# Performance work log

Measured on AMD Instinct MI355X. Metric: run time of the kernel, lower is better.

The kernel has to match this reference:

```python
import jax, jax.numpy as jnp
import numpy as np

BIG = 1e6  # sentinel 'no zero pixel found yet' distance; BIG**2 = 1e12 fits fp32


def _edt(is_fg):
    """Exact Euclidean distance transform (scipy.distance_transform_edt semantics):
    distance from each nonzero pixel to the nearest zero pixel. is_fg: [N,H,W] bool.
    Separable exact algorithm: 1D vertical distance-to-zero per column via cummax
    scans, then min-plus convolution with the parabola (j-k)^2 along rows."""
    N, H, W = is_fg.shape
    is_zero = ~is_fg
    ih = jnp.arange(H, dtype=jnp.float32)[None, :, None]
    # nearest zero at-or-above / at-or-below along H (per column)
    up = jax.lax.cummax(jnp.where(is_zero, ih, -BIG), axis=1)
    dn = -jax.lax.cummax(jnp.where(is_zero, -ih, -BIG), axis=1, reverse=True)
    g = jnp.minimum(ih - up, dn - ih)               # [N,H,W] vertical 1D distance
    g2 = jnp.minimum(g, BIG) ** 2
    ks = jnp.arange(W, dtype=jnp.float32)
    def col(j):
        # exact 2D squared distance for output column j: min_k (j-k)^2 + g(.,.,k)^2
        return jnp.min((j.astype(jnp.float32) - ks) ** 2 + g2, axis=-1)  # [N,H]
    d2 = jax.lax.map(col, jnp.arange(W))            # [W,N,H], sequential -> low memory
    return jnp.sqrt(jnp.moveaxis(d2, 0, -1))        # [N,H,W]


def setup_inputs() -> dict:
    key = jax.random.key(0)
    k1, k2 = jax.random.split(key)
    B, C, H, W = 8, 12, 256, 256
    logits = jax.random.normal(k1, (B, C, H, W), dtype=jnp.float32)
    targets = jax.random.randint(k2, (B, H, W), 0, C, dtype=jnp.int32)
    return {"logits": logits, "targets": targets}


def reference(logits, targets):
    B, C, H, W = logits.shape
    probs = jax.nn.softmax(logits, axis=1)                                  # [B,C,H,W]
    gt = targets[:, None, :, :] == jnp.arange(C, dtype=targets.dtype)[None, :, None, None]
    m = gt.reshape(B * C, H, W)
    pos = _edt(m)          # distance inside foreground to nearest background
    neg = _edt(~m)         # distance inside background to nearest foreground
    dt = (neg - pos).reshape(B, C, H, W)
    has_fg = gt.any(axis=(2, 3))                                            # [B,C]
    dt = jnp.where(has_fg[:, :, None, None], dt, 0.0)
    # per-image, per-class min-max normalization (matches torch view(B,-1).min/max)
    dmin = dt.min(axis=(2, 3), keepdims=True)
    dmax = dt.max(axis=(2, 3), keepdims=True)
    dt = (dt - dmin) / (dmax - dmin + 1e-8)
    inter = jnp.sum(probs * dt, axis=(2, 3))                                # [B,C]
    denom = jnp.sum(probs * probs, axis=(2, 3)) + jnp.sum(dt * dt, axis=(2, 3)) + 1e-6
    dice = 2.0 * inter / denom
    # sum_c mean_b (1-dice) / C  == mean over (b,c) since ignore_index=255 is out of range
    return jnp.mean(1.0 - dice)
```

## Files before the change

### kernel.cpp

```cpp
#include <hip/hip_runtime.h>
#include <math.h>

constexpr int B_  = 8;
constexpr int C_  = 12;
constexpr int H_  = 256;
constexpr int W_  = 256;
constexpr int HW_ = H_ * W_;
constexpr int NBC_ = B_ * C_;
constexpr int VB_  = NBC_ * 4;
constexpr int SMB_ = B_ * (HW_ / 1024);
constexpr int PADL_ = 128;
constexpr int LROW_ = PADL_ + W_ + PADL_;


__global__ void __launch_bounds__(256) k_vp(
                     const int* __restrict__ t,
                     const float* __restrict__ logits,
                     unsigned short* __restrict__ gpk,
                     int* __restrict__ hasfg_p,
                     float2* __restrict__ den,
                     float* __restrict__ out) {
    int tid = threadIdx.x;
    if (blockIdx.x >= VB_) {
        int pb = blockIdx.x - VB_;
        int b = pb >> 6;
        int p = ((pb & 63) << 10) + tid * 4;
        const float* lb = logits + (size_t)b * C_ * HW_ + p;
        float4 l[C_];
        float4 mx = make_float4(-3.4e38f, -3.4e38f, -3.4e38f, -3.4e38f);
        #pragma unroll
        for (int c = 0; c < C_; ++c) {
            l[c] = *(const float4*)(lb + (size_t)c * HW_);
            mx.x = fmaxf(mx.x, l[c].x);
            mx.y = fmaxf(mx.y, l[c].y);
            mx.z = fmaxf(mx.z, l[c].z);
            mx.w = fmaxf(mx.w, l[c].w);
        }
        float4 s = make_float4(0.f, 0.f, 0.f, 0.f);
        #pragma unroll
        for (int c = 0; c < C_; ++c) {
            s.x += __expf(l[c].x - mx.x);
            s.y += __expf(l[c].y - mx.y);
            s.z += __expf(l[c].z - mx.z);
            s.w += __expf(l[c].w - mx.w);
        }
        float2* dp = den + (size_t)b * HW_ + p;
        ((float4*)dp)[0] = make_float4(mx.x, 1.0f / s.x, mx.y, 1.0f / s.y);
        ((float4*)dp)[1] = make_float4(mx.z, 1.0f / s.z, mx.w, 1.0f / s.w);
        return;
    }

    if (blockIdx.x == 0 && tid == 0) out[0] = 0.0f;
    constexpr int SEG = 8, SH = 32;
    int s  = tid >> 5;
    int wl = tid & 31;
    int blk = blockIdx.x;
    int bc = blk >> 2;
    int w0 = (blk & 3) * 64;
    int b = bc / C_, c = bc - b * C_;
    int w = w0 + 2 * wl;
    const int* base = t + b * HW_ + w;
    int h0 = s * SH;

    unsigned tp0[SH / 4], tp1[SH / 4];
    int le0 = -1, ln0 = -1, fe0 = 256, fn0 = 256;
    int le1 = -1, ln1 = -1, fe1 = 256, fn1 = 256;
    #pragma unroll
    for (int i = 0; i < SH; ++i) {
        int2 tv = *(const int2*)(base + (h0 + i) * W_);
        if ((i & 3) == 0) { tp0[i >> 2] = 0; tp1[i >> 2] = 0; }
        tp0[i >> 2] |= (unsigned)tv.x << ((i & 3) * 8);
        tp1[i >> 2] |= (unsigned)tv.y << ((i & 3) * 8);
        int h = h0 + i;
        if (tv.x == c) { le0 = h; if (fe0 == 256) fe0 = h; }
        else           { ln0 = h; if (fn0 == 256) fn0 = h; }
        if (tv.y == c) { le1 = h; if (fe1 == 256) fe1 = h; }
        else           { ln1 = h; if (fn1 == 256) fn1 = h; }
    }
    __shared__ int sLE[SEG][64], sLN[SEG][64], sFE[SEG][64], sFN[SEG][64];
    sLE[s][2 * wl] = le0; sLE[s][2 * wl + 1] = le1;
    sLN[s][2 * wl] = ln0; sLN[s][2 * wl + 1] = ln1;
    sFE[s][2 * wl] = fe0; sFE[s][2 * wl + 1] = fe1;
    sFN[s][2 * wl] = fn0; sFN[s][2 * wl + 1] = fn1;
    __syncthreads();

    int carLE0 = -1, carLN0 = -1, carLE1 = -1, carLN1 = -1;
    for (int q = 0; q < s; ++q) {
        carLE0 = max(carLE0, sLE[q][2 * wl]);
        carLN0 = max(carLN0, sLN[q][2 * wl]);
        carLE1 = max(carLE1, sLE[q][2 * wl + 1]);
        carLN1 = max(carLN1, sLN[q][2 * wl + 1]);
    }
    int carFE0 = 256, carFN0 = 256, carFE1 = 256, carFN1 = 256;
    for (int q = s + 1; q < SEG; ++q) {
        carFE0 = min(carFE0, sFE[q][2 * wl]);
        carFN0 = min(carFN0, sFN[q][2 * wl]);
        carFE1 = min(carFE1, sFE[q][2 * wl + 1]);
        carFN1 = min(carFN1, sFN[q][2 * wl + 1]);
    }

    bool pred = false;
    if (tid < 64) {
        int m = -1;
        #pragma unroll
        for (int q = 0; q < SEG; ++q) m = max(m, sLE[q][tid]);
        pred = (m >= 0);
    }
    bool anyfg = __any(pred);
    if (tid == 0) hasfg_p[blk] = anyfg ? 1 : 0;

    unsigned ap0[SH / 4], ap1[SH / 4];
    {
        int l0 = carLE0, n0 = carLN0, l1 = carLE1, n1 = carLN1;
        #pragma unroll
        for (int i = 0; i < SH; ++i) {
            int h = h0 + i;
            int tv0 = (tp0[i >> 2] >> ((i & 3) * 8)) & 0xFF;
            int tv1 = (tp1[i >> 2] >> ((i & 3) * 8)) & 0xFF;
            int lz0, lz1;
            if (tv0 == c) { l0 = h; lz0 = n0; } else { n0 = h; lz0 = l0; }
            if (tv1 == c) { l1 = h; lz1 = n1; } else { n1 = h; lz1 = l1; }
            unsigned a0 = (lz0 < 0) ? 255u : (unsigned)(h - lz0 - 1);
            unsigned a1 = (lz1 < 0) ? 255u : (unsigned)(h - lz1 - 1);
            if ((i & 3) == 0) { ap0[i >> 2] = 0; ap1[i >> 2] = 0; }
            ap0[i >> 2] |= a0 << ((i & 3) * 8);
            ap1[i >> 2] |= a1 << ((i & 3) * 8);
        }
    }
    {
        int fe0_ = carFE0, fn0_ = carFN0, fe1_ = carFE1, fn1_ = carFN1;
        unsigned* gk32 = (unsigned*)(gpk + (size_t)bc * HW_ + w);
        #pragma unroll
        for (int i = SH - 1; i >= 0; --i) {
            int h = h0 + i;
            int tv0 = (tp0[i >> 2] >> ((i & 3) * 8)) & 0xFF;
            int tv1 = (tp1[i >> 2] >> ((i & 3) * 8)) & 0xFF;
            int nz0, nz1; bool fg0, fg1;
            if (tv0 == c) { fe0_ = h; fg0 = true;  nz0 = fn0_; }
            else          { fn0_ = h; fg0 = false; nz0 = fe0_; }
            if (tv1 == c) { fe1_ = h; fg1 = true;  nz1 = fn1_; }
            else          { fn1_ = h; fg1 = false; nz1 = fe1_; }
            unsigned au0 = (ap0[i >> 2] >> ((i & 3) * 8)) & 0xFF;
            unsigned au1 = (ap1[i >> 2] >> ((i & 3) * 8)) & 0xFF;
            int dl0 = (au0 == 255u) ? 0x7FFF : (int)au0 + 1;
            int dl1 = (au1 == 255u) ? 0x7FFF : (int)au1 + 1;
            int dn0 = (nz0 > 255) ? 0x7FFF : (nz0 - h);
            int dn1 = (nz1 > 255) ? 0x7FFF : (nz1 - h);
            unsigned d0 = (unsigned)min(dl0, dn0) | (fg0 ? 0x8000u : 0u);
            unsigned d1 = (unsigned)min(dl1, dn1) | (fg1 ? 0x8000u : 0u);
            gk32[(h * W_) >> 1] = d0 | (d1 << 16);
        }
    }
}

__global__ void __launch_bounds__(256) k_edt(
                      const unsigned short* __restrict__ gpk,
                      const float* __restrict__ logits,
                      const float2* __restrict__ den,
                      const int* __restrict__ hasfg_p,
                      float* __restrict__ part) {
    __shared__ float sp[4][LROW_];
    __shared__ float sn[4][LROW_];
    int wave = threadIdx.x >> 6;
    int lane = threadIdx.x & 63;
    int row = blockIdx.x * 4 + wave;
    int bc = row >> 8;
    int b = bc / C_, c = bc - b * C_;
    int h = row & (H_ - 1);

    int hfl = 0;
    if (lane < 4) hfl = hasfg_p[bc * 4 + lane];
    bool hf = __any(hfl != 0);

    const float*  lrow = logits + ((size_t)b * C_ + c) * HW_ + h * W_;
    const float2* drow = den + (size_t)b * HW_ + h * W_;
    float lv[4]; float2 mv[4];
    #pragma unroll
    for (int i = 0; i < 4; ++i) {
        int j = lane + 64 * i;
        lv[i] = lrow[j];
        mv[i] = drow[j];
    }

    float dv[4];
    if (hf) {
        const ushort4 v4 = ((const ushort4*)(gpk + (size_t)row * W_))[lane];

        float4 inf4 = make_float4(3.0e38f, 3.0e38f, 3.0e38f, 3.0e38f);
        int slot = (lane < 32) ? lane : (lane + 64);
        ((float4*)&sp[wave][0])[slot] = inf4;
        ((float4*)&sn[wave][0])[slot] = inf4;

        float s1 = (float)(1000000 - h);
        float sent2 = s1 * s1;
        float4 fpv, fnv;
        {
            const unsigned short* vs = (const unsigned short*)&v4;
            float* fp = (float*)&fpv;
            float* fn = (float*)&fnv;
            #pragma unroll
            for (int q = 0; q < 4; ++q) {
                unsigned v = vs[q];
                unsigned d = v & 0x7FFFu;
                float g2 = (d == 0x7FFFu) ? sent2 : (float)(d * d);
                bool fg = (v & 0x8000u) != 0;
                fp[q] = fg ? g2 : 0.0f;
                fn[q] = fg ? 0.0f : g2;
            }
        }
        ((float4*)&sp[wave][PADL_])[lane] = fpv;
        ((float4*)&sn[wave][PADL_])[lane] = fnv;
        asm volatile("s_waitcnt lgkmcnt(0)" ::: "memory");

        float bp[4], bn[4];
        #pragma unroll
        for (int i = 0; i < 4; ++i) {
            int j = PADL_ + lane + 64 * i;
            bp[i] = sp[wave][j];
            bn[i] = sn[wave][j];
        }
        {
            bool doneN = false;
            int r = 1;
            for (; r <= PADL_; ++r) {
                float fr = (float)r;
                float r2 = fr * fr;
                float m = fmaxf(fmaxf(bn[0], bn[1]), fmaxf(bn[2], bn[3]));
                if (!__any(r2 < m)) { doneN = true; break; }
                #pragma unroll
                for (int i = 0; i < 4; ++i) {
                    int j = PADL_ + lane + 64 * i;
                    float v = fminf(sn[wave][j - r], sn[wave][j + r]);
                    bn[i] = fminf(bn[i], fmaf(fr, fr, v));
                }
            }
            if (!doneN) {
                for (; r < W_; ++r) {
                    float fr = (float)r;
                    float r2 = fr * fr;
                    float m = fmaxf(fmaxf(bn[0], bn[1]), fmaxf(bn[2], bn[3]));
                    if (!__any(r2 < m)) break;
                    #pragma unroll
                    for (int i = 0; i < 4; ++i) {
                        int j = PADL_ + lane + 64 * i;
                        int jm = max(j - r, 0);
                        int jp = min(j + r, LROW_ - 1);
                        float v = fminf(sn[wave][jm], sn[wave][jp]);
                        bn[i] = fminf(bn[i], fmaf(fr, fr, v));
                    }
                }
            }
        }
        {
            bool doneP = false;
            int r = 1;
            for (; r <= PADL_; ++r) {
                float fr = (float)r;
                float r2 = fr * fr;
                float m = fmaxf(fmaxf(bp[0], bp[1]), fmaxf(bp[2], bp[3]));
                if (!__any(r2 < m)) { doneP = true; break; }
                #pragma unroll
                for (int i = 0; i < 4; ++i) {
                    int j = PADL_ + lane + 64 * i;
                    float v = fminf(sp[wave][j - r], sp[wave][j + r]);
                    bp[i] = fminf(bp[i], fmaf(fr, fr, v));
                }
            }
            if (!doneP) {
                for (; r < W_; ++r) {
                    float fr = (float)r;
                    float r2 = fr * fr;
                    float m = fmaxf(fmaxf(bp[0], bp[1]), fmaxf(bp[2], bp[3]));
                    if (!__any(r2 < m)) break;
                    #pragma unroll
                    for (int i = 0; i < 4; ++i) {
                        int j = PADL_ + lane + 64 * i;
                        int jm = max(j - r, 0);
                        int jp = min(j + r, LROW_ - 1);
                        float v = fminf(sp[wave][jm], sp[wave][jp]);
                        bp[i] = fminf(bp[i], fmaf(fr, fr, v));
                    }
                }
            }
        }
        #pragma unroll
        for (int i = 0; i < 4; ++i) dv[i] = sqrtf(bn[i]) - sqrtf(bp[i]);
    } else {
        #pragma unroll
        for (int i = 0; i < 4; ++i) dv[i] = 0.0f;
    }

    float s_pd = 0.f, s_p = 0.f, s_pp = 0.f, s_d = 0.f, s_dd = 0.f;
    float mn = 3.4e38f, mx = -3.4e38f;
    #pragma unroll
    for (int i = 0; i < 4; ++i) {
        float2 mi = mv[i];
        float pr = __expf(lv[i] - mi.x) * mi.y;
        float d = dv[i];
        s_pd = fmaf(pr, d, s_pd);
        s_p += pr;
        s_pp = fmaf(pr, pr, s_pp);
        s_d += d;
        s_dd = fmaf(d, d, s_dd);
        mn = fminf(mn, d);
        mx = fmaxf(mx, d);
    }
    #pragma unroll
    for (int off = 32; off; off >>= 1) {
        s_pd += __shfl_down(s_pd, off);
        s_p  += __shfl_down(s_p, off);
        s_pp += __shfl_down(s_pp, off);
        s_d  += __shfl_down(s_d, off);
        s_dd += __shfl_down(s_dd, off);
        mn = fminf(mn, __shfl_down(mn, off));
        mx = fmaxf(mx, __shfl_down(mx, off));
    }
    if (lane == 0) {
        float4* p4 = (float4*)(part + (size_t)row * 8);
        p4[0] = make_float4(s_pd, s_p, s_pp, s_d);
        p4[1] = make_float4(s_dd, mn, mx, 0.0f);
    }
}

__global__ void __launch_bounds__(256) k_bcred(
                       const float* __restrict__ part, float* __restrict__ out) {
    int bc = blockIdx.x;
    int tid = threadIdx.x;
    const float4* p4 = (const float4*)(part + ((size_t)bc * 256 + tid) * 8);
    float4 a = p4[0], bq = p4[1];
    float s_pd = a.x, s_p = a.y, s_pp = a.z;
    float s_d = a.w, s_dd = bq.x, mn = bq.y, mx = bq.z;
    #pragma unroll
    for (int off = 32; off; off >>= 1) {
        s_pd += __shfl_down(s_pd, off);
        s_p  += __shfl_down(s_p, off);
        s_pp += __shfl_down(s_pp, off);
        s_d  += __shfl_down(s_d, off);
        s_dd += __shfl_down(s_dd, off);
        mn = fminf(mn, __shfl_down(mn, off));
        mx = fmaxf(mx, __shfl_down(mx, off));
    }
    __shared__ float red[4][7];
    int wave = tid >> 6, lane = tid & 63;
    if (lane == 0) {
        red[wave][0] = s_pd; red[wave][1] = s_p; red[wave][2] = s_pp;
        red[wave][3] = s_d;  red[wave][4] = s_dd; red[wave][5] = mn; red[wave][6] = mx;
    }
    __syncthreads();
    if (tid == 0) {
        s_pd = red[0][0]; s_p = red[0][1]; s_pp = red[0][2];
        s_d = red[0][3]; s_dd = red[0][4]; mn = red[0][5]; mx = red[0][6];
        for (int w = 1; w < 4; ++w) {
            s_pd += red[w][0]; s_p += red[w][1]; s_pp += red[w][2];
            s_d += red[w][3]; s_dd += red[w][4];
            mn = fminf(mn, red[w][5]); mx = fmaxf(mx, red[w][6]);
        }
        float sc = 1.0f / (mx - mn + 1e-8f);
        float inter = sc * (s_pd - mn * s_p);
        float d2 = sc * sc * (s_dd - 2.0f * mn * s_d + mn * mn * (float)HW_);
        float dice = 2.0f * inter / (s_pp + d2 + 1e-6f);
        atomicAdd(out, (1.0f - dice) * (1.0f / (float)NBC_));
    }
}

extern "C" void kernel_launch(void* const* d_in, const int* in_sizes, int n_in,
                              void* d_out, int out_size, void* d_ws, size_t ws_size,
                              hipStream_t stream) {
    const float* logits  = (const float*)d_in[0];
    const int*   targets = (const int*)d_in[1];
    float* out = (float*)d_out;

    unsigned short* gpk = (unsigned short*)d_ws;
    int* hasfg_p = (int*)(gpk + (size_t)NBC_ * HW_);
    float* part = (float*)(hasfg_p + NBC_ * 8);
    float2* den = (float2*)(part + (size_t)NBC_ * H_ * 8);

    k_vp<<<VB_ + SMB_, 256, 0, stream>>>(targets, logits, gpk,
                                         hasfg_p, den, out);
    k_edt<<<NBC_ * H_ / 4, 256, 0, stream>>>(gpk, logits, den, hasfg_p, part);
    k_bcred<<<NBC_, 256, 0, stream>>>(part, out);
}
```

Baseline: 110.3 us.

## Split fused vertical-scan/softmax kernel into two kernels with finer work decomposition

Separates the combined vertical distance pass and softmax-stat pass into two kernels, k_vert and k_sm. k_vert now uses 512-thread blocks with 16 segments of 16 rows and one column per thread, up from 8 segments of 32 rows and two columns per thread. k_sm processes 2 pixels per thread across twice as many blocks. This is meant to increase parallelism and cut per-thread register pressure, at the cost of an extra kernel launch, 16-bit instead of 32-bit stores, and losing the overlap of the two workloads inside a single grid.

```diff
diff --git a/kernel.cpp b/kernel.cpp
--- a/kernel.cpp
+++ b/kernel.cpp
@@ -7,100 +7,59 @@
 constexpr int W_  = 256;
 constexpr int HW_ = H_ * W_;
 constexpr int NBC_ = B_ * C_;
-constexpr int VB_  = NBC_ * 4;
-constexpr int SMB_ = B_ * (HW_ / 1024);
+constexpr int VB_  = NBC_ * 8;
+constexpr int SMB_ = B_ * (HW_ / 512);
 constexpr int PADL_ = 128;
 constexpr int LROW_ = PADL_ + W_ + PADL_;
 
 
-__global__ void __launch_bounds__(256) k_vp(
+__global__ void __launch_bounds__(512) k_vert(
                      const int* __restrict__ t,
-                     const float* __restrict__ logits,
                      unsigned short* __restrict__ gpk,
                      int* __restrict__ hasfg_p,
-                     float2* __restrict__ den,
                      float* __restrict__ out) {
     int tid = threadIdx.x;
-    if (blockIdx.x >= VB_) {
-        int pb = blockIdx.x - VB_;
-        int b = pb >> 6;
-        int p = ((pb & 63) << 10) + tid * 4;
-        const float* lb = logits + (size_t)b * C_ * HW_ + p;
-        float4 l[C_];
-        float4 mx = make_float4(-3.4e38f, -3.4e38f, -3.4e38f, -3.4e38f);
-        #pragma unroll
-        for (int c = 0; c < C_; ++c) {
-            l[c] = *(const float4*)(lb + (size_t)c * HW_);
-            mx.x = fmaxf(mx.x, l[c].x);
-            mx.y = fmaxf(mx.y, l[c].y);
-            mx.z = fmaxf(mx.z, l[c].z);
-            mx.w = fmaxf(mx.w, l[c].w);
-        }
-        float4 s = make_float4(0.f, 0.f, 0.f, 0.f);
-        #pragma unroll
-        for (int c = 0; c < C_; ++c) {
-            s.x += __expf(l[c].x - mx.x);
-            s.y += __expf(l[c].y - mx.y);
-            s.z += __expf(l[c].z - mx.z);
-            s.w += __expf(l[c].w - mx.w);
-        }
-        float2* dp = den + (size_t)b * HW_ + p;
-        ((float4*)dp)[0] = make_float4(mx.x, 1.0f / s.x, mx.y, 1.0f / s.y);
-        ((float4*)dp)[1] = make_float4(mx.z, 1.0f / s.z, mx.w, 1.0f / s.w);
-        return;
-    }
-
     if (blockIdx.x == 0 && tid == 0) out[0] = 0.0f;
-    constexpr int SEG = 8, SH = 32;
+    constexpr int SEG = 16, SH = 16;
     int s  = tid >> 5;
     int wl = tid & 31;
     int blk = blockIdx.x;
-    int bc = blk >> 2;
-    int w0 = (blk & 3) * 64;
+    int bc = blk >> 3;
+    int w0 = (blk & 7) * 32;
     int b = bc / C_, c = bc - b * C_;
-    int w = w0 + 2 * wl;
+    int w = w0 + wl;
     const int* base = t + b * HW_ + w;
     int h0 = s * SH;
 
-    unsigned tp0[SH / 4], tp1[SH / 4];
-    int le0 = -1, ln0 = -1, fe0 = 256, fn0 = 256;
-    int le1 = -1, ln1 = -1, fe1 = 256, fn1 = 256;
+    unsigned tp[SH / 4];
+    int lastEq = -1, lastNeq = -1, firstEq = 256, firstNeq = 256;
     #pragma unroll
     for (int i = 0; i < SH; ++i) {
-        int2 tv = *(const int2*)(base + (h0 + i) * W_);
-        if ((i & 3) == 0) { tp0[i >> 2] = 0; tp1[i >> 2] = 0; }
-        tp0[i >> 2] |= (unsigned)tv.x << ((i & 3) * 8);
-        tp1[i >> 2] |= (unsigned)tv.y << ((i & 3) * 8);
+        int tv = base[(h0 + i) * W_];
+        if ((i & 3) == 0) tp[i >> 2] = 0;
+        tp[i >> 2] |= (unsigned)tv << ((i & 3) * 8);
         int h = h0 + i;
-        if (tv.x == c) { le0 = h; if (fe0 == 256) fe0 = h; }
-        else           { ln0 = h; if (fn0 == 256) fn0 = h; }
-        if (tv.y == c) { le1 = h; if (fe1 == 256) fe1 = h; }
-        else           { ln1 = h; if (fn1 == 256) fn1 = h; }
-    }
-    __shared__ int sLE[SEG][64], sLN[SEG][64], sFE[SEG][64], sFN[SEG][64];
-    sLE[s][2 * wl] = le0; sLE[s][2 * wl + 1] = le1;
-    sLN[s][2 * wl] = ln0; sLN[s][2 * wl + 1] = ln1;
-    sFE[s][2 * wl] = fe0; sFE[s][2 * wl + 1] = fe1;
-    sFN[s][2 * wl] = fn0; sFN[s][2 * wl + 1] = fn1;
+        if (tv == c) { lastEq = h;  if (firstEq  == 256) firstEq  = h; }
+        else         { lastNeq = h; if (firstNeq == 256) firstNeq = h; }
+    }
+    __shared__ int sLE[SEG][32], sLN[SEG][32], sFE[SEG][32], sFN[SEG][32];
+    sLE[s][wl] = lastEq; sLN[s][wl] = lastNeq;
+    sFE[s][wl] = firstEq; sFN[s][wl] = firstNeq;
     __syncthreads();
 
-    int carLE0 = -1, carLN0 = -1, carLE1 = -1, carLN1 = -1;
+    int carLE = -1, carLN = -1;
     for (int q = 0; q < s; ++q) {
-        carLE0 = max(carLE0, sLE[q][2 * wl]);
-        carLN0 = max(carLN0, sLN[q][2 * wl]);
-        carLE1 = max(carLE1, sLE[q][2 * wl + 1]);
-        carLN1 = max(carLN1, sLN[q][2 * wl + 1]);
-    }
-    int carFE0 = 256, carFN0 = 256, carFE1 = 256, carFN1 = 256;
+        carLE = max(carLE, sLE[q][wl]);
+        carLN = max(carLN, sLN[q][wl]);
+    }
+    int carFE = 256, carFN = 256;
     for (int q = s + 1; q < SEG; ++q) {
-        carFE0 = min(carFE0, sFE[q][2 * wl]);
-        carFN0 = min(carFN0, sFN[q][2 * wl]);
-        carFE1 = min(carFE1, sFE[q][2 * wl + 1]);
-        carFN1 = min(carFN1, sFN[q][2 * wl + 1]);
+        carFE = min(carFE, sFE[q][wl]);
+        carFN = min(carFN, sFN[q][wl]);
     }
 
     bool pred = false;
-    if (tid < 64) {
+    if (tid < 32) {
         int m = -1;
         #pragma unroll
         for (int q = 0; q < SEG; ++q) m = max(m, sLE[q][tid]);
@@ -109,48 +68,63 @@
     bool anyfg = __any(pred);
     if (tid == 0) hasfg_p[blk] = anyfg ? 1 : 0;
 
-    unsigned ap0[SH / 4], ap1[SH / 4];
+    unsigned ap[SH / 4];
     {
-        int l0 = carLE0, n0 = carLN0, l1 = carLE1, n1 = carLN1;
+        int le = carLE, ln = carLN;
         #pragma unroll
         for (int i = 0; i < SH; ++i) {
             int h = h0 + i;
-            int tv0 = (tp0[i >> 2] >> ((i & 3) * 8)) & 0xFF;
-            int tv1 = (tp1[i >> 2] >> ((i & 3) * 8)) & 0xFF;
-            int lz0, lz1;
-            if (tv0 == c) { l0 = h; lz0 = n0; } else { n0 = h; lz0 = l0; }
-            if (tv1 == c) { l1 = h; lz1 = n1; } else { n1 = h; lz1 = l1; }
-            unsigned a0 = (lz0 < 0) ? 255u : (unsigned)(h - lz0 - 1);
-            unsigned a1 = (lz1 < 0) ? 255u : (unsigned)(h - lz1 - 1);
-            if ((i & 3) == 0) { ap0[i >> 2] = 0; ap1[i >> 2] = 0; }
-            ap0[i >> 2] |= a0 << ((i & 3) * 8);
-            ap1[i >> 2] |= a1 << ((i & 3) * 8);
+            int tv = (tp[i >> 2] >> ((i & 3) * 8)) & 0xFF;
+            int lz;
+            if (tv == c) { le = h; lz = ln; } else { ln = h; lz = le; }
+            unsigned a = (lz < 0) ? 255u : (unsigned)(h - lz - 1);
+            if ((i & 3) == 0) ap[i >> 2] = 0;
+            ap[i >> 2] |= a << ((i & 3) * 8);
         }
     }
     {
-        int fe0_ = carFE0, fn0_ = carFN0, fe1_ = carFE1, fn1_ = carFN1;
-        unsigned* gk32 = (unsigned*)(gpk + (size_t)bc * HW_ + w);
+        int fe = carFE, fn = carFN;
+        unsigned short* gk = gpk + (size_t)bc * HW_ + w;
         #pragma unroll
         for (int i = SH - 1; i >= 0; --i) {
             int h = h0 + i;
-            int tv0 = (tp0[i >> 2] >> ((i & 3) * 8)) & 0xFF;
-            int tv1 = (tp1[i >> 2] >> ((i & 3) * 8)) & 0xFF;
-            int nz0, nz1; bool fg0, fg1;
-            if (tv0 == c) { fe0_ = h; fg0 = true;  nz0 = fn0_; }
-            else          { fn0_ = h; fg0 = false; nz0 = fe0_; }
-            if (tv1 == c) { fe1_ = h; fg1 = true;  nz1 = fn1_; }
-            else          { fn1_ = h; fg1 = false; nz1 = fe1_; }
-            unsigned au0 = (ap0[i >> 2] >> ((i & 3) * 8)) & 0xFF;
-            unsigned au1 = (ap1[i >> 2] >> ((i & 3) * 8)) & 0xFF;
-            int dl0 = (au0 == 255u) ? 0x7FFF : (int)au0 + 1;
-            int dl1 = (au1 == 255u) ? 0x7FFF : (int)au1 + 1;
-            int dn0 = (nz0 > 255) ? 0x7FFF : (nz0 - h);
-            int dn1 = (nz1 > 255) ? 0x7FFF : (nz1 - h);
-            unsigned d0 = (unsigned)min(dl0, dn0) | (fg0 ? 0x8000u : 0u);
-            unsigned d1 = (unsigned)min(dl1, dn1) | (fg1 ? 0x8000u : 0u);
-            gk32[(h * W_) >> 1] = d0 | (d1 << 16);
-        }
-    }
+            int tv = (tp[i >> 2] >> ((i & 3) * 8)) & 0xFF;
+            int nz; bool fg;
+            if (tv == c) { fe = h; fg = true;  nz = fn; }
+            else         { fn = h; fg = false; nz = fe; }
+            unsigned au = (ap[i >> 2] >> ((i & 3) * 8)) & 0xFF;
+            int dl  = (au == 255u) ? 0x7FFF : (int)au + 1;
+            int dnx = (nz > 255) ? 0x7FFF : (nz - h);
+            int d = min(dl, dnx);
+            gk[h * W_] = (unsigned short)(d | (fg ? 0x8000 : 0));
+        }
+    }
+}
+
+__global__ void __launch_bounds__(256) k_sm(
+                     const float* __restrict__ logits,
+                     float2* __restrict__ den) {
+    int tid = threadIdx.x;
+    int pb = blockIdx.x;
+    int b = pb >> 7;
+    int p = ((pb & 127) << 9) + tid * 2;
+    const float* lb = logits + (size_t)b * C_ * HW_ + p;
+    float2 l[C_];
+    float mxx = -3.4e38f, mxy = -3.4e38f;
+    #pragma unroll
+    for (int c = 0; c < C_; ++c) {
+        l[c] = *(const float2*)(lb + (size_t)c * HW_);
+        mxx = fmaxf(mxx, l[c].x);
+        mxy = fmaxf(mxy, l[c].y);
+    }
+    float sx = 0.f, sy = 0.f;
+    #pragma unroll
+    for (int c = 0; c < C_; ++c) {
+        sx += __expf(l[c].x - mxx);
+        sy += __expf(l[c].y - mxy);
+    }
+    *(float4*)(den + (size_t)b * HW_ + p) =
+        make_float4(mxx, 1.0f / sx, mxy, 1.0f / sy);
 }
 
 __global__ void __launch_bounds__(256) k_edt(
@@ -169,7 +143,7 @@
     int h = row & (H_ - 1);
 
     int hfl = 0;
-    if (lane < 4) hfl = hasfg_p[bc * 4 + lane];
+    if (lane < 8) hfl = hasfg_p[bc * 8 + lane];
     bool hf = __any(hfl != 0);
 
     const float*  lrow = logits + ((size_t)b * C_ + c) * HW_ + h * W_;
@@ -375,8 +349,8 @@
     float* part = (float*)(hasfg_p + NBC_ * 8);
     float2* den = (float2*)(part + (size_t)NBC_ * H_ * 8);
 
-    k_vp<<<VB_ + SMB_, 256, 0, stream>>>(targets, logits, gpk,
-                                         hasfg_p, den, out);
+    k_vert<<<VB_, 512, 0, stream>>>(targets, gpk, hasfg_p, out);
+    k_sm<<<SMB_, 256, 0, stream>>>(logits, den);
     k_edt<<<NBC_ * H_ / 4, 256, 0, stream>>>(gpk, logits, den, hasfg_p, part);
     k_bcred<<<NBC_, 256, 0, stream>>>(part, out);
 }
```

Result: faster. 106.4 us (-3.6%).
